# Kernel tuning notes

Hardware: AMD Instinct MI355X
Metric: run time of the kernel (lower is better)

## Reference

```python
import jax, jax.numpy as jnp
import numpy as np

N_HEAD = 8
DK = 32  # q_k_dim
DV = 32  # v_dim
INF = 1e9


def _rope(x, cos, sin):
    # x: [BP, L, H, DK]; cos/sin: [BP, L, 1, DK//2]
    xr = x.reshape(x.shape[:-1] + (DK // 2, 2))
    re, im = xr[..., 0], xr[..., 1]
    out_re = re * cos - im * sin
    out_im = re * sin + im * cos
    return jnp.stack([out_re, out_im], axis=-1).reshape(x.shape)


def setup_inputs() -> dict:
    key = jax.random.key(0)
    ks = jax.random.split(key, 12)
    B, PN, PL, NV, DM = 8, 8, 511, 2, 512
    D = N_HEAD * DV  # 256
    x = jax.random.normal(ks[0], (B, PN, PL, NV), dtype=jnp.float32)
    # irregular but increasing time stamps per patch (length PL+1)
    t = jnp.sort(jax.random.uniform(ks[1], (B, PN, PL + 1), dtype=jnp.float32) * 100.0, axis=-1)
    mask = jax.random.randint(ks[2], (B, PN, PL + 1), 0, 2).astype(jnp.int32)
    s_in = 1.0 / np.sqrt(NV)
    s_d = 1.0 / np.sqrt(D)
    return {
        "x": x,
        "t": t,
        "mask": mask,
        "emb_token": jnp.zeros((1, 1, 1, NV), dtype=jnp.float32),
        "Wq": jax.random.normal(ks[3], (NV, N_HEAD * DK), dtype=jnp.float32) * s_in,
        "Wk": jax.random.normal(ks[4], (NV, N_HEAD * DK), dtype=jnp.float32) * s_in,
        "Wv": jax.random.normal(ks[5], (NV, N_HEAD * DV), dtype=jnp.float32) * s_in,
        "Wo": jax.random.normal(ks[6], (D, DM), dtype=jnp.float32) * s_d,
        "ln_g": jnp.ones((D,), dtype=jnp.float32),
        "ln_b": jnp.zeros((D,), dtype=jnp.float32),
        "W1": jax.random.normal(ks[7], (D, 4 * D), dtype=jnp.float32) * s_d,
        "b1": jnp.zeros((4 * D,), dtype=jnp.float32),
        "W2": jax.random.normal(ks[8], (4 * D, D), dtype=jnp.float32) * (1.0 / np.sqrt(4 * D)),
        "b2": jnp.zeros((D,), dtype=jnp.float32),
    }


def reference(x, t, mask, emb_token, Wq, Wk, Wv, Wo, ln_g, ln_b, W1, b1, W2, b2):
    B, PN, PL, NV = x.shape
    L = PL + 1
    BP = B * PN
    # prepend learned embedding token
    emb = jnp.broadcast_to(emb_token, (B, PN, 1, NV))
    xx = jnp.concatenate([emb, x], axis=2)  # [B, PN, L, NV]
    Q = (xx @ Wq).reshape(BP, L, N_HEAD, DK)
    K = (xx @ Wk).reshape(BP, L, N_HEAD, DK)
    V = (xx @ Wv).reshape(BP, L, N_HEAD, DV)
    # irregular time-based RoPE
    thetas = 1.0 / (1000.0 ** (jnp.arange(0, DK, 2, dtype=jnp.float32) / DK))  # [DK//2]
    freqs = t.reshape(BP, L)[:, :, None] * thetas  # [BP, L, DK//2]
    cos = jnp.cos(freqs)[:, :, None, :]
    sin = jnp.sin(freqs)[:, :, None, :]
    Q = _rope(Q, cos, sin)
    K = _rope(K, cos, sin)
    Qh = Q.transpose(0, 2, 1, 3)  # [BP, H, L, DK]
    Kh = K.transpose(0, 2, 1, 3)
    Vh = V.transpose(0, 2, 1, 3)
    scale = np.sqrt(float(DK))
    scores = jnp.einsum('bhqd,bhkd->bhqk', Qh / scale, Kh)  # [BP, H, L, L]
    m = mask.reshape(BP, L)
    mmat = (m[:, :, None] * m[:, None, :])[:, None, :, :]  # [BP, 1, L, L]
    scores = jnp.where(mmat == 0, -INF, scores)
    attn = jax.nn.softmax(scores, axis=-1)
    out = jnp.einsum('bhqk,bhkd->bhqd', attn, Vh)  # [BP, H, L, DV]
    last = out[:, :, 0, :].reshape(B, PN, N_HEAD * DV)  # take emb-token query
    # FFN residual (dropout disabled / eval mode)
    h = jax.nn.relu(last @ W1 + b1) @ W2 + b2
    y = last + h
    mu = jnp.mean(y, axis=-1, keepdims=True)
    var = jnp.var(y, axis=-1, keepdims=True)
    yn = (y - mu) / jnp.sqrt(var + 1e-5) * ln_g + ln_b
    return yn @ Wo  # [B, PN, d_model]
```

## Files before the change

kernel.cpp:

```cpp
#include <hip/hip_runtime.h>
#include <math.h>

namespace {
constexpr int L   = 512;
constexpr int D   = 256;
constexpr int DM  = 512;
constexpr int HID = 1024;
constexpr float INV_SQRT_DK = 0.17677669529663687f;

__device__ __constant__ float THETA[16] = {
  1.0f,           0.64938163f,  0.42169650f,  0.27384196f,
  0.17782794f,    0.11547820f,  0.074989421f, 0.048696753f,
  0.031622777f,   0.020535250f, 0.013335214f, 0.0086596432f,
  0.0056234133f,  0.0036517412f,0.0023713737f,0.0015399265f };

__global__ __launch_bounds__(512, 2)
void k_attn(const float* __restrict__ x, const float* __restrict__ t,
            const int* __restrict__ mask, const float* __restrict__ emb,
            const float* __restrict__ Wq, const float* __restrict__ Wk,
            const float* __restrict__ Wv, float* __restrict__ last) {
  const int bp = blockIdx.x & 63, h = blockIdx.x >> 6;
  const int tid = threadIdx.x, lane = tid & 63, wid = tid >> 6;

  __shared__ float wk0[32], wk1[32], wv0[32], wv1[32];
  __shared__ float red[24];

  if (tid < 32) {
    wk0[tid] = Wk[h * 32 + tid]; wk1[tid] = Wk[256 + h * 32 + tid];
    wv0[tid] = Wv[h * 32 + tid]; wv1[tid] = Wv[256 + h * 32 + tid];
  }

  const int   m0 = mask[bp * L];
  const float tl = t[bp * L + tid];
  const int   ml = mask[bp * L + tid];
  float xl0, xl1;
  if (tid == 0) { xl0 = emb[0]; xl1 = emb[1]; }
  else {
    float2 v = reinterpret_cast<const float2*>(x)[bp * (L - 1) + tid - 1];
    xl0 = v.x; xl1 = v.y;
  }

  float cj[16], sj[16];
  #pragma unroll
  for (int j = 0; j < 16; ++j) __sincosf(tl * THETA[j], &sj[j], &cj[j]);

  float qre = 0.f, qim = 0.f;
  if (lane < 16) {
    const float t0v = t[bp * L];
    const float e0 = emb[0], e1 = emb[1];
    const float re = e0 * Wq[h * 32 + 2 * lane]     + e1 * Wq[256 + h * 32 + 2 * lane];
    const float im = e0 * Wq[h * 32 + 2 * lane + 1] + e1 * Wq[256 + h * 32 + 2 * lane + 1];
    float s0, c0;
    __sincosf(t0v * THETA[lane], &s0, &c0);
    qre = (re * c0 - im * s0) * INV_SQRT_DK;
    qim = (re * s0 + im * c0) * INV_SQRT_DK;
  }
  __syncthreads();

  float sc = 0.f;
  #pragma unroll
  for (int j = 0; j < 16; ++j) {
    const int c = 2 * j;
    const float xr  = xl0 * wk0[c]     + xl1 * wk1[c];
    const float xi  = xl0 * wk0[c + 1] + xl1 * wk1[c + 1];
    const float kre = xr * cj[j] - xi * sj[j];
    const float kim = xr * sj[j] + xi * cj[j];
    sc += __shfl(qre, j) * kre + __shfl(qim, j) * kim;
  }

  const float e = (m0 == 0) ? 1.f : (ml ? __expf(sc) : 0.f);

  float se = e, s0a = e * xl0, s1a = e * xl1;
  #pragma unroll
  for (int o = 32; o; o >>= 1) {
    se  += __shfl_xor(se, o);
    s0a += __shfl_xor(s0a, o);
    s1a += __shfl_xor(s1a, o);
  }
  if (lane == 0) { red[wid] = se; red[8 + wid] = s0a; red[16 + wid] = s1a; }
  __syncthreads();
  se = 0.f; s0a = 0.f; s1a = 0.f;
  #pragma unroll
  for (int w = 0; w < 8; ++w) { se += red[w]; s0a += red[8 + w]; s1a += red[16 + w]; }

  if (tid < 32) last[bp * 256 + h * 32 + tid] = (s0a * wv0[tid] + s1a * wv1[tid]) / se;
}

__global__ __launch_bounds__(512, 1)
void k_ffn(const float* __restrict__ last, const float* __restrict__ W1,
           const float* __restrict__ b1, const float* __restrict__ W2,
           float* __restrict__ partial) {
  const int kt = blockIdx.x & 15, mt = blockIdx.x >> 4;
  const int tid = threadIdx.x, lane = tid & 63, w = tid >> 6;

  __shared__ float ls[4][256];
  __shared__ float s_p1[8][4][64];
  __shared__ float hs[4][64];
  __shared__ float s_p2[8][4][256];

  #pragma unroll
  for (int q = 0; q < 2; ++q) {
    const int idx = tid + q * 512;
    ls[idx >> 8][idx & 255] = last[(mt * 4 + (idx >> 8)) * 256 + (idx & 255)];
  }
  __syncthreads();

  const int j = kt * 64 + lane;
  {
    const float* w1p = W1 + (size_t)(w * 32) * HID + j;
    float a0 = 0.f, a1 = 0.f, a2 = 0.f, a3 = 0.f;
    #pragma unroll
    for (int g = 0; g < 8; ++g) {
      const float4 l0 = *reinterpret_cast<const float4*>(&ls[0][w * 32 + g * 4]);
      const float4 l1 = *reinterpret_cast<const float4*>(&ls[1][w * 32 + g * 4]);
      const float4 l2 = *reinterpret_cast<const float4*>(&ls[2][w * 32 + g * 4]);
      const float4 l3 = *reinterpret_cast<const float4*>(&ls[3][w * 32 + g * 4]);
      const float w_0 = w1p[(g * 4 + 0) * HID];
      const float w_1 = w1p[(g * 4 + 1) * HID];
      const float w_2 = w1p[(g * 4 + 2) * HID];
      const float w_3 = w1p[(g * 4 + 3) * HID];
      a0 = fmaf(l0.x, w_0, a0); a0 = fmaf(l0.y, w_1, a0);
      a0 = fmaf(l0.z, w_2, a0); a0 = fmaf(l0.w, w_3, a0);
      a1 = fmaf(l1.x, w_0, a1); a1 = fmaf(l1.y, w_1, a1);
      a1 = fmaf(l1.z, w_2, a1); a1 = fmaf(l1.w, w_3, a1);
      a2 = fmaf(l2.x, w_0, a2); a2 = fmaf(l2.y, w_1, a2);
      a2 = fmaf(l2.z, w_2, a2); a2 = fmaf(l2.w, w_3, a2);
      a3 = fmaf(l3.x, w_0, a3); a3 = fmaf(l3.y, w_1, a3);
      a3 = fmaf(l3.z, w_2, a3); a3 = fmaf(l3.w, w_3, a3);
    }
    s_p1[w][0][lane] = a0; s_p1[w][1][lane] = a1;
    s_p1[w][2][lane] = a2; s_p1[w][3][lane] = a3;
  }
  __syncthreads();

  if (tid < 256) {
    const int r = tid >> 6, k = tid & 63;
    float h = b1[kt * 64 + k];
    #pragma unroll
    for (int ww = 0; ww < 8; ++ww) h += s_p1[ww][r][k];
    hs[r][k] = fmaxf(h, 0.f);
  }
  __syncthreads();

  {
    float hr[4][8];
    #pragma unroll
    for (int r = 0; r < 4; ++r) {
      *reinterpret_cast<float4*>(&hr[r][0]) = *reinterpret_cast<const float4*>(&hs[r][w * 8]);
      *reinterpret_cast<float4*>(&hr[r][4]) = *reinterpret_cast<const float4*>(&hs[r][w * 8 + 4]);
    }
    float4 c0 = {0,0,0,0}, c1 = {0,0,0,0}, c2 = {0,0,0,0}, c3 = {0,0,0,0};
    const float* w2p = W2 + (size_t)(kt * 64 + w * 8) * D + lane * 4;
    #pragma unroll
    for (int k = 0; k < 8; ++k) {
      const float4 wv = *reinterpret_cast<const float4*>(w2p + (size_t)k * D);
      c0.x = fmaf(hr[0][k], wv.x, c0.x); c0.y = fmaf(hr[0][k], wv.y, c0.y);
      c0.z = fmaf(hr[0][k], wv.z, c0.z); c0.w = fmaf(hr[0][k], wv.w, c0.w);
      c1.x = fmaf(hr[1][k], wv.x, c1.x); c1.y = fmaf(hr[1][k], wv.y, c1.y);
      c1.z = fmaf(hr[1][k], wv.z, c1.z); c1.w = fmaf(hr[1][k], wv.w, c1.w);
      c2.x = fmaf(hr[2][k], wv.x, c2.x); c2.y = fmaf(hr[2][k], wv.y, c2.y);
      c2.z = fmaf(hr[2][k], wv.z, c2.z); c2.w = fmaf(hr[2][k], wv.w, c2.w);
      c3.x = fmaf(hr[3][k], wv.x, c3.x); c3.y = fmaf(hr[3][k], wv.y, c3.y);
      c3.z = fmaf(hr[3][k], wv.z, c3.z); c3.w = fmaf(hr[3][k], wv.w, c3.w);
    }
    *reinterpret_cast<float4*>(&s_p2[w][0][lane * 4]) = c0;
    *reinterpret_cast<float4*>(&s_p2[w][1][lane * 4]) = c1;
    *reinterpret_cast<float4*>(&s_p2[w][2][lane * 4]) = c2;
    *reinterpret_cast<float4*>(&s_p2[w][3][lane * 4]) = c3;
  }
  __syncthreads();

  {
    const int r = tid >> 7, c0i = (tid & 127) * 2;
    float v0 = 0.f, v1 = 0.f;
    #pragma unroll
    for (int ww = 0; ww < 8; ++ww) {
      v0 += s_p2[ww][r][c0i];
      v1 += s_p2[ww][r][c0i + 1];
    }
    *reinterpret_cast<float2*>(
        &partial[(size_t)(kt * 64 + mt * 4 + r) * 256 + c0i]) = make_float2(v0, v1);
  }
}

__global__ __launch_bounds__(512, 1)
void k_tail(const float* __restrict__ last, const float* __restrict__ partial,
            const float* __restrict__ b2, const float* __restrict__ ln_g,
            const float* __restrict__ ln_b, const float* __restrict__ Wo,
            float* __restrict__ out) {
  const int ct = blockIdx.x & 3, bp = blockIdx.x >> 2;
  const int tid = threadIdx.x, lane = tid & 63, wid = tid >> 6;

  __shared__ float s_y[2][256];
  __shared__ float s_yn[256];
  __shared__ float s_op[8][128];
  __shared__ float red[8];

  {
    const int col = tid & 255, khh = tid >> 8;
    float acc = khh ? 0.f : (last[bp * 256 + col] + b2[col]);
    #pragma unroll
    for (int kt = khh * 8; kt < khh * 8 + 8; ++kt)
      acc += partial[(size_t)(kt * 64 + bp) * 256 + col];
    s_y[khh][col] = acc;
  }
  __syncthreads();

  float y = 0.f;
  if (tid < 256) y = s_y[0][tid] + s_y[1][tid];
  float ssum = (tid < 256) ? y : 0.f, ssq = (tid < 256) ? y * y : 0.f;
  #pragma unroll
  for (int o = 32; o; o >>= 1) { ssum += __shfl_xor(ssum, o); ssq += __shfl_xor(ssq, o); }
  if (tid < 256 && lane == 0) { red[wid] = ssum; red[4 + wid] = ssq; }
  __syncthreads();
  ssum = red[0] + red[1] + red[2] + red[3];
  ssq  = red[4] + red[5] + red[6] + red[7];
  const float mu   = ssum / 256.f;
  const float var  = ssq / 256.f - mu * mu;
  const float rstd = rsqrtf(var + 1e-5f);
  if (tid < 256) s_yn[tid] = (y - mu) * rstd * ln_g[tid] + ln_b[tid];
  __syncthreads();

  {
    const int l6 = tid & 63, kq = tid >> 6;
    const int c0 = ct * 128 + 2 * l6;
    float f0 = 0.f, f1 = 0.f;
    #pragma unroll 8
    for (int i = kq * 32; i < kq * 32 + 32; ++i) {
      const float2 wv = *reinterpret_cast<const float2*>(&Wo[(size_t)i * DM + c0]);
      const float yv = s_yn[i];
      f0 = fmaf(yv, wv.x, f0);
      f1 = fmaf(yv, wv.y, f1);
    }
    s_op[kq][2 * l6] = f0; s_op[kq][2 * l6 + 1] = f1;
  }
  __syncthreads();
  if (tid < 128) {
    float a = 0.f;
    #pragma unroll
    for (int kq = 0; kq < 8; ++kq) a += s_op[kq][tid];
    out[(size_t)bp * DM + ct * 128 + tid] = a;
  }
}
}

extern "C" void kernel_launch(void* const* d_in, const int* in_sizes, int n_in,
                              void* d_out, int out_size, void* d_ws, size_t ws_size,
                              hipStream_t stream) {
  const float* x    = (const float*)d_in[0];
  const float* t    = (const float*)d_in[1];
  const int*   mask = (const int*)  d_in[2];
  const float* emb  = (const float*)d_in[3];
  const float* Wq   = (const float*)d_in[4];
  const float* Wk   = (const float*)d_in[5];
  const float* Wv   = (const float*)d_in[6];
  const float* Wo   = (const float*)d_in[7];
  const float* lng  = (const float*)d_in[8];
  const float* lnb  = (const float*)d_in[9];
  const float* W1   = (const float*)d_in[10];
  const float* b1   = (const float*)d_in[11];
  const float* W2   = (const float*)d_in[12];
  const float* b2   = (const float*)d_in[13];
  float* out = (float*)d_out;

  float* ws      = (float*)d_ws;
  float* last    = ws;
  float* partial = ws + 16384;

  k_attn<<<512, 512, 0, stream>>>(x, t, mask, emb, Wq, Wk, Wv, last);
  k_ffn <<<256, 512, 0, stream>>>(last, W1, b1, W2, partial);
  k_tail<<<256, 512, 0, stream>>>(last, partial, b2, lng, lnb, Wo, out);
}
```

Measured before the change: 19.14 us.

## Fold query into key weights algebraically and prefetch FFN/output weights into registers

In the attention kernel, the emb-token query is folded into the key projection weights, giving four per-head coefficient vectors. Each key's score then becomes a short sin/cos dot product instead of rebuilding the rotated key and shuffling q. The FFN and tail kernels issue their W1, W2 and Wo global loads into register arrays at kernel start, before the barriers and dependent work. That lets weight fetch latency overlap with the activation loads and reductions, at the cost of higher register pressure.

```diff
diff --git a/kernel.cpp b/kernel.cpp
--- a/kernel.cpp
+++ b/kernel.cpp
@@ -22,13 +22,9 @@
   const int bp = blockIdx.x & 63, h = blockIdx.x >> 6;
   const int tid = threadIdx.x, lane = tid & 63, wid = tid >> 6;
 
-  __shared__ float wk0[32], wk1[32], wv0[32], wv1[32];
+  __shared__ float s_q[32];
+  __shared__ float s_pq[4][16];
   __shared__ float red[24];
-
-  if (tid < 32) {
-    wk0[tid] = Wk[h * 32 + tid]; wk1[tid] = Wk[256 + h * 32 + tid];
-    wv0[tid] = Wv[h * 32 + tid]; wv1[tid] = Wv[256 + h * 32 + tid];
-  }
 
   const int   m0 = mask[bp * L];
   const float tl = t[bp * L + tid];
@@ -36,37 +32,42 @@
   float xl0, xl1;
   if (tid == 0) { xl0 = emb[0]; xl1 = emb[1]; }
   else {
-    float2 v = reinterpret_cast<const float2*>(x)[bp * (L - 1) + tid - 1];
+    const float2 v = reinterpret_cast<const float2*>(x)[bp * (L - 1) + tid - 1];
     xl0 = v.x; xl1 = v.y;
   }
 
-  float cj[16], sj[16];
-  #pragma unroll
-  for (int j = 0; j < 16; ++j) __sincosf(tl * THETA[j], &sj[j], &cj[j]);
-
-  float qre = 0.f, qim = 0.f;
-  if (lane < 16) {
+  if (tid < 16) {
     const float t0v = t[bp * L];
     const float e0 = emb[0], e1 = emb[1];
-    const float re = e0 * Wq[h * 32 + 2 * lane]     + e1 * Wq[256 + h * 32 + 2 * lane];
-    const float im = e0 * Wq[h * 32 + 2 * lane + 1] + e1 * Wq[256 + h * 32 + 2 * lane + 1];
+    const float re = e0 * Wq[h * 32 + 2 * tid]     + e1 * Wq[256 + h * 32 + 2 * tid];
+    const float im = e0 * Wq[h * 32 + 2 * tid + 1] + e1 * Wq[256 + h * 32 + 2 * tid + 1];
     float s0, c0;
-    __sincosf(t0v * THETA[lane], &s0, &c0);
-    qre = (re * c0 - im * s0) * INV_SQRT_DK;
-    qim = (re * s0 + im * c0) * INV_SQRT_DK;
-  }
-  __syncthreads();
-
-  float sc = 0.f;
+    __sincosf(t0v * THETA[tid], &s0, &c0);
+    s_q[tid]      = (re * c0 - im * s0) * INV_SQRT_DK;
+    s_q[16 + tid] = (re * s0 + im * c0) * INV_SQRT_DK;
+  }
+  __syncthreads();
+  if (tid < 16) {
+    const int j = tid;
+    const float qre = s_q[j], qim = s_q[16 + j];
+    const float k0  = Wk[h * 32 + 2 * j],       k01 = Wk[h * 32 + 2 * j + 1];
+    const float k1  = Wk[256 + h * 32 + 2 * j], k11 = Wk[256 + h * 32 + 2 * j + 1];
+    s_pq[0][j] = qre * k0 + qim * k01;
+    s_pq[1][j] = qre * k1 + qim * k11;
+    s_pq[2][j] = qim * k0 - qre * k01;
+    s_pq[3][j] = qim * k1 - qre * k11;
+  }
+  __syncthreads();
+
+  float A = 0.f, B = 0.f;
   #pragma unroll
   for (int j = 0; j < 16; ++j) {
-    const int c = 2 * j;
-    const float xr  = xl0 * wk0[c]     + xl1 * wk1[c];
-    const float xi  = xl0 * wk0[c + 1] + xl1 * wk1[c + 1];
-    const float kre = xr * cj[j] - xi * sj[j];
-    const float kim = xr * sj[j] + xi * cj[j];
-    sc += __shfl(qre, j) * kre + __shfl(qim, j) * kim;
-  }
+    float sn, cs;
+    __sincosf(tl * THETA[j], &sn, &cs);
+    A = fmaf(cs, s_pq[0][j], A); A = fmaf(sn, s_pq[2][j], A);
+    B = fmaf(cs, s_pq[1][j], B); B = fmaf(sn, s_pq[3][j], B);
+  }
+  const float sc = xl0 * A + xl1 * B;
 
   const float e = (m0 == 0) ? 1.f : (ml ? __expf(sc) : 0.f);
 
@@ -83,7 +84,9 @@
   #pragma unroll
   for (int w = 0; w < 8; ++w) { se += red[w]; s0a += red[8 + w]; s1a += red[16 + w]; }
 
-  if (tid < 32) last[bp * 256 + h * 32 + tid] = (s0a * wv0[tid] + s1a * wv1[tid]) / se;
+  if (tid < 32)
+    last[bp * 256 + h * 32 + tid] =
+        (s0a * Wv[h * 32 + tid] + s1a * Wv[256 + h * 32 + tid]) / se;
 }
 
 __global__ __launch_bounds__(512, 1)
@@ -98,6 +101,14 @@
   __shared__ float hs[4][64];
   __shared__ float s_p2[8][4][256];
 
+  const int j = kt * 64 + lane;
+  float w1r[32];
+  {
+    const float* w1p = W1 + (size_t)(w * 32) * HID + j;
+    #pragma unroll
+    for (int g = 0; g < 32; ++g) w1r[g] = w1p[(size_t)g * HID];
+  }
+
   #pragma unroll
   for (int q = 0; q < 2; ++q) {
     const int idx = tid + q * 512;
@@ -105,9 +116,7 @@
   }
   __syncthreads();
 
-  const int j = kt * 64 + lane;
-  {
-    const float* w1p = W1 + (size_t)(w * 32) * HID + j;
+  {
     float a0 = 0.f, a1 = 0.f, a2 = 0.f, a3 = 0.f;
     #pragma unroll
     for (int g = 0; g < 8; ++g) {
@@ -115,30 +124,34 @@
       const float4 l1 = *reinterpret_cast<const float4*>(&ls[1][w * 32 + g * 4]);
       const float4 l2 = *reinterpret_cast<const float4*>(&ls[2][w * 32 + g * 4]);
       const float4 l3 = *reinterpret_cast<const float4*>(&ls[3][w * 32 + g * 4]);
-      const float w_0 = w1p[(g * 4 + 0) * HID];
-      const float w_1 = w1p[(g * 4 + 1) * HID];
-      const float w_2 = w1p[(g * 4 + 2) * HID];
-      const float w_3 = w1p[(g * 4 + 3) * HID];
-      a0 = fmaf(l0.x, w_0, a0); a0 = fmaf(l0.y, w_1, a0);
-      a0 = fmaf(l0.z, w_2, a0); a0 = fmaf(l0.w, w_3, a0);
-      a1 = fmaf(l1.x, w_0, a1); a1 = fmaf(l1.y, w_1, a1);
-      a1 = fmaf(l1.z, w_2, a1); a1 = fmaf(l1.w, w_3, a1);
-      a2 = fmaf(l2.x, w_0, a2); a2 = fmaf(l2.y, w_1, a2);
-      a2 = fmaf(l2.z, w_2, a2); a2 = fmaf(l2.w, w_3, a2);
-      a3 = fmaf(l3.x, w_0, a3); a3 = fmaf(l3.y, w_1, a3);
-      a3 = fmaf(l3.z, w_2, a3); a3 = fmaf(l3.w, w_3, a3);
+      a0 = fmaf(l0.x, w1r[g*4+0], a0); a0 = fmaf(l0.y, w1r[g*4+1], a0);
+      a0 = fmaf(l0.z, w1r[g*4+2], a0); a0 = fmaf(l0.w, w1r[g*4+3], a0);
+      a1 = fmaf(l1.x, w1r[g*4+0], a1); a1 = fmaf(l1.y, w1r[g*4+1], a1);
+      a1 = fmaf(l1.z, w1r[g*4+2], a1); a1 = fmaf(l1.w, w1r[g*4+3], a1);
+      a2 = fmaf(l2.x, w1r[g*4+0], a2); a2 = fmaf(l2.y, w1r[g*4+1], a2);
+      a2 = fmaf(l2.z, w1r[g*4+2], a2); a2 = fmaf(l2.w, w1r[g*4+3], a2);
+      a3 = fmaf(l3.x, w1r[g*4+0], a3); a3 = fmaf(l3.y, w1r[g*4+1], a3);
+      a3 = fmaf(l3.z, w1r[g*4+2], a3); a3 = fmaf(l3.w, w1r[g*4+3], a3);
     }
     s_p1[w][0][lane] = a0; s_p1[w][1][lane] = a1;
     s_p1[w][2][lane] = a2; s_p1[w][3][lane] = a3;
   }
+
+  float4 w2r[8];
+  {
+    const float* w2p = W2 + (size_t)(kt * 64 + w * 8) * D + lane * 4;
+    #pragma unroll
+    for (int k = 0; k < 8; ++k)
+      w2r[k] = *reinterpret_cast<const float4*>(w2p + (size_t)k * D);
+  }
   __syncthreads();
 
   if (tid < 256) {
     const int r = tid >> 6, k = tid & 63;
-    float h = b1[kt * 64 + k];
-    #pragma unroll
-    for (int ww = 0; ww < 8; ++ww) h += s_p1[ww][r][k];
-    hs[r][k] = fmaxf(h, 0.f);
+    float hv = b1[kt * 64 + k];
+    #pragma unroll
+    for (int ww = 0; ww < 8; ++ww) hv += s_p1[ww][r][k];
+    hs[r][k] = fmaxf(hv, 0.f);
   }
   __syncthreads();
 
@@ -150,10 +163,9 @@
       *reinterpret_cast<float4*>(&hr[r][4]) = *reinterpret_cast<const float4*>(&hs[r][w * 8 + 4]);
     }
     float4 c0 = {0,0,0,0}, c1 = {0,0,0,0}, c2 = {0,0,0,0}, c3 = {0,0,0,0};
-    const float* w2p = W2 + (size_t)(kt * 64 + w * 8) * D + lane * 4;
     #pragma unroll
     for (int k = 0; k < 8; ++k) {
-      const float4 wv = *reinterpret_cast<const float4*>(w2p + (size_t)k * D);
+      const float4 wv = w2r[k];
       c0.x = fmaf(hr[0][k], wv.x, c0.x); c0.y = fmaf(hr[0][k], wv.y, c0.y);
       c0.z = fmaf(hr[0][k], wv.z, c0.z); c0.w = fmaf(hr[0][k], wv.w, c0.w);
       c1.x = fmaf(hr[1][k], wv.x, c1.x); c1.y = fmaf(hr[1][k], wv.y, c1.y);
@@ -196,6 +208,16 @@
   __shared__ float s_op[8][128];
   __shared__ float red[8];
 
+  const int l6 = tid & 63, kq = tid >> 6;
+  const int c0 = ct * 128 + 2 * l6;
+  float2 wor[32];
+  {
+    const float* wop = Wo + (size_t)(kq * 32) * DM + c0;
+    #pragma unroll
+    for (int i = 0; i < 32; ++i)
+      wor[i] = *reinterpret_cast<const float2*>(wop + (size_t)i * DM);
+  }
+
   {
     const int col = tid & 255, khh = tid >> 8;
     float acc = khh ? 0.f : (last[bp * 256 + col] + b2[col]);
@@ -222,15 +244,12 @@
   __syncthreads();
 
   {
-    const int l6 = tid & 63, kq = tid >> 6;
-    const int c0 = ct * 128 + 2 * l6;
     float f0 = 0.f, f1 = 0.f;
-    #pragma unroll 8
-    for (int i = kq * 32; i < kq * 32 + 32; ++i) {
-      const float2 wv = *reinterpret_cast<const float2*>(&Wo[(size_t)i * DM + c0]);
-      const float yv = s_yn[i];
-      f0 = fmaf(yv, wv.x, f0);
-      f1 = fmaf(yv, wv.y, f1);
+    #pragma unroll
+    for (int i = 0; i < 32; ++i) {
+      const float yv = s_yn[kq * 32 + i];
+      f0 = fmaf(yv, wor[i].x, f0);
+      f1 = fmaf(yv, wor[i].y, f1);
     }
     s_op[kq][2 * l6] = f0; s_op[kq][2 * l6 + 1] = f1;
   }
@@ -238,7 +257,7 @@
   if (tid < 128) {
     float a = 0.f;
     #pragma unroll
-    for (int kq = 0; kq < 8; ++kq) a += s_op[kq][tid];
+    for (int k = 0; k < 8; ++k) a += s_op[k][tid];
     out[(size_t)bp * DM + ct * 128 + tid] = a;
   }
 }
```

Result: no change. 18.87 us (-1.4%).
